# Kernel tuning notes

Measured on AMD Instinct MI355X. Metric: run time of the kernel, lower is better.

The kernel has to match this reference:

```python
import jax, jax.numpy as jnp
import numpy as np

N_WIRES = 22
DEPTH = 1


def _apply_ry(state, theta, wire):
    # RY(theta) = [[cos(t/2), -sin(t/2)], [sin(t/2), cos(t/2)]] (torchquantum convention)
    c = jnp.cos(theta * 0.5).astype(jnp.complex64)
    s = jnp.sin(theta * 0.5).astype(jnp.complex64)
    st = jnp.moveaxis(state, wire, 0)  # [2, 2^(n-1) ...]
    new = jnp.stack([c * st[0] - s * st[1], s * st[0] + c * st[1]])
    return jnp.moveaxis(new, 0, wire)


def _apply_cnot(state, ctrl, tgt):
    st = jnp.moveaxis(state, (ctrl, tgt), (0, 1))
    st = st.at[1].set(st[1, ::-1])  # flip target where control == 1
    return jnp.moveaxis(st, (0, 1), (ctrl, tgt))


def _encode(angles, n_wires=N_WIRES, depth=DEPTH):
    # start in |0...0>
    state = jnp.zeros((2,) * n_wires, dtype=jnp.complex64).at[(0,) * n_wires].set(1.0 + 0.0j)
    for w in range(n_wires):
        state = _apply_ry(state, angles[w], w)
    for _ in range(depth):
        for i in range(n_wires):
            state = _apply_cnot(state, i, (i + 1) % n_wires)
    return state


def setup_inputs() -> dict:
    key = jax.random.key(0)
    kx, ky = jax.random.split(key)
    x = jax.random.normal(kx, (N_WIRES,), dtype=jnp.float32)
    y = jax.random.normal(ky, (N_WIRES,), dtype=jnp.float32)
    return {"x": x, "y": y}


def reference(x, y):
    n = N_WIRES
    psi_x = _encode(x)  # state1 in the torch code
    psi_y = _encode(y)
    # torch does: states_y @ states_x.conj() on tensors of shape [1, 2, ..., 2]
    # -> batched 2x2 matmul over the leading n-1 qubit axes, then abs().view(-1)
    shape = (1,) + (2,) * n
    overlap = jnp.matmul(psi_y.reshape(shape), jnp.conj(psi_x).reshape(shape))
    return jnp.abs(overlap).reshape(-1)
```

## Files before the change

### kernel.cpp

```cpp
#include <hip/hip_runtime.h>
#include <math.h>


#define N_WIRES 22

__global__ __launch_bounds__(256) void quantum_overlap_kernel(
    const float* __restrict__ x, const float* __restrict__ y,
    float* __restrict__ out)
{
    __shared__ float fx[2 * N_WIRES];
    __shared__ float fy[2 * N_WIRES];
    const int t = threadIdx.x;
    if (t < N_WIRES) {
        float sv, cv;
        sincosf(0.5f * x[t], &sv, &cv);
        fx[2 * t] = cv; fx[2 * t + 1] = sv;
        sincosf(0.5f * y[t], &sv, &cv);
        fy[2 * t] = cv; fy[2 * t + 1] = sv;
    }
    __syncthreads();

    const unsigned b = blockIdx.x * 256u + (unsigned)t;

    float coreX = 1.0f, coreY = 1.0f;
#pragma unroll
    for (int k = 2; k <= 19; ++k) {
        unsigned bit = ((b >> (19 - k)) ^ (b >> (20 - k))) & 1u;
        coreX *= fx[2 * k + bit];
        coreY *= fy[2 * k + bit];
    }

    const unsigned s0  = (b >> 19) & 1u;
    const unsigned s1  = (b >> 18) & 1u;
    const unsigned s19 = b & 1u;

    float X[2][2], Y[2][2];
#pragma unroll
    for (int i20 = 0; i20 < 2; ++i20) {
#pragma unroll
        for (int i21 = 0; i21 < 2; ++i21) {
            unsigned a0  = s0 ^ (unsigned)i21;
            unsigned a1  = s1 ^ s0 ^ (unsigned)i21;
            unsigned a20 = (unsigned)i20 ^ s19;
            unsigned a21 = (unsigned)i21 ^ (unsigned)i20;
            float gX = fx[a0] * fx[2 + a1] * fx[40 + a20] * fx[42 + a21];
            float gY = fy[a0] * fy[2 + a1] * fy[40 + a20] * fy[42 + a21];
            X[i20][i21] = coreX * gX;
            Y[i20][i21] = coreY * gY;
        }
    }

    float4 o;
    o.x = fabsf(Y[0][0] * X[0][0] + Y[0][1] * X[1][0]);
    o.y = fabsf(Y[0][0] * X[0][1] + Y[0][1] * X[1][1]);
    o.z = fabsf(Y[1][0] * X[0][0] + Y[1][1] * X[1][0]);
    o.w = fabsf(Y[1][0] * X[0][1] + Y[1][1] * X[1][1]);
    reinterpret_cast<float4*>(out)[b] = o;
}

extern "C" void kernel_launch(void* const* d_in, const int* in_sizes, int n_in,
                              void* d_out, int out_size, void* d_ws, size_t ws_size,
                              hipStream_t stream) {
    const float* x = (const float*)d_in[0];
    const float* y = (const float*)d_in[1];
    float* out = (float*)d_out;
    const unsigned n_b = 1u << 20;
    quantum_overlap_kernel<<<n_b / 256, 256, 0, stream>>>(x, y, out);
}
```

Baseline: 64.38 us.

## Factor product-state amplitudes into precomputed half tables plus 2x2 overlap lookup

Adds a small precompute kernel that builds 512-entry partial-product tables for the two halves of the middle qubits of each state, plus an 8-entry table of the absolute 2x2 overlap factors. The main kernel then forms each output from a Gray-code index, two table lookups per state, and a float4 broadcast, instead of an 18-term product chain plus per-thread gate math. This cuts ALU work in a kernel that writes 16 MB, at the price of an extra launch and a dependency on workspace memory. It also relies on pulling the common core factor out of the absolute value.

Result: no change. 63.95 us (-0.7%).

```diff
diff --git a/kernel.cpp b/kernel.cpp
--- a/kernel.cpp
+++ b/kernel.cpp
@@ -2,59 +2,70 @@
 #include <math.h>
 
 
-#define N_WIRES 22
-
-__global__ __launch_bounds__(256) void quantum_overlap_kernel(
+__global__ __launch_bounds__(256) void qk_precompute(
     const float* __restrict__ x, const float* __restrict__ y,
-    float* __restrict__ out)
+    float* __restrict__ ws)
 {
-    __shared__ float fx[2 * N_WIRES];
-    __shared__ float fy[2 * N_WIRES];
+    __shared__ float f[2][44];
     const int t = threadIdx.x;
-    if (t < N_WIRES) {
+    if (t < 22) {
         float sv, cv;
         sincosf(0.5f * x[t], &sv, &cv);
-        fx[2 * t] = cv; fx[2 * t + 1] = sv;
+        f[0][2 * t] = cv; f[0][2 * t + 1] = sv;
         sincosf(0.5f * y[t], &sv, &cv);
-        fy[2 * t] = cv; fy[2 * t + 1] = sv;
+        f[1][2 * t] = cv; f[1][2 * t + 1] = sv;
     }
     __syncthreads();
 
-    const unsigned b = blockIdx.x * 256u + (unsigned)t;
+    const int e   = blockIdx.x * 256 + t;
+    const int tbl = e >> 9;
+    const int i   = e & 511;
+    const float* F = f[tbl & 1];
+    float prod = 1.0f;
+    if (tbl < 2) {
+#pragma unroll
+        for (int q = 0; q < 9; ++q) prod *= F[2 * (10 - q) + ((i >> q) & 1)];
+    } else {
+#pragma unroll
+        for (int p = 0; p < 9; ++p) prod *= F[2 * (19 - p) + ((i >> p) & 1)];
+    }
+    ws[e] = prod;
 
-    float coreX = 1.0f, coreY = 1.0f;
+    if (blockIdx.x == 0 && t < 8) {
+        const int s0 = (t >> 2) & 1, s1 = (t >> 1) & 1, s19 = t & 1;
 #pragma unroll
-    for (int k = 2; k <= 19; ++k) {
-        unsigned bit = ((b >> (19 - k)) ^ (b >> (20 - k))) & 1u;
-        coreX *= fx[2 * k + bit];
-        coreY *= fy[2 * k + bit];
-    }
-
-    const unsigned s0  = (b >> 19) & 1u;
-    const unsigned s1  = (b >> 18) & 1u;
-    const unsigned s19 = b & 1u;
-
-    float X[2][2], Y[2][2];
+        for (int ii = 0; ii < 2; ++ii) {
 #pragma unroll
-    for (int i20 = 0; i20 < 2; ++i20) {
+            for (int j = 0; j < 2; ++j) {
+                float sum = 0.0f;
 #pragma unroll
-        for (int i21 = 0; i21 < 2; ++i21) {
-            unsigned a0  = s0 ^ (unsigned)i21;
-            unsigned a1  = s1 ^ s0 ^ (unsigned)i21;
-            unsigned a20 = (unsigned)i20 ^ s19;
-            unsigned a21 = (unsigned)i21 ^ (unsigned)i20;
-            float gX = fx[a0] * fx[2 + a1] * fx[40 + a20] * fx[42 + a21];
-            float gY = fy[a0] * fy[2 + a1] * fy[40 + a20] * fy[42 + a21];
-            X[i20][i21] = coreX * gX;
-            Y[i20][i21] = coreY * gY;
+                for (int k = 0; k < 2; ++k) {
+                    float kx = f[0][s0 ^ j] * f[0][2 + (s1 ^ s0 ^ j)]
+                             * f[0][40 + (k ^ s19)] * f[0][42 + (j ^ k)];
+                    float ky = f[1][s0 ^ k] * f[1][2 + (s1 ^ s0 ^ k)]
+                             * f[1][40 + (ii ^ s19)] * f[1][42 + (k ^ ii)];
+                    sum += ky * kx;
+                }
+                ws[2048 + 4 * t + 2 * ii + j] = fabsf(sum);
+            }
         }
     }
+}
 
+__global__ __launch_bounds__(256) void qk_main(
+    const float* __restrict__ ws, float* __restrict__ out)
+{
+    const unsigned b  = blockIdx.x * 256u + threadIdx.x;
+    const unsigned g  = b ^ (b >> 1);
+    const unsigned i2 = g & 511u;
+    const unsigned i1 = (g >> 9) & 511u;
+    const float coreX = ws[i1]        * ws[1024u + i2];
+    const float coreY = ws[512u + i1] * ws[1536u + i2];
+    const float p = fabsf(coreX * coreY);
+    const unsigned m = ((b >> 17) & 6u) | (b & 1u);
+    const float4 a = reinterpret_cast<const float4*>(ws + 2048)[m];
     float4 o;
-    o.x = fabsf(Y[0][0] * X[0][0] + Y[0][1] * X[1][0]);
-    o.y = fabsf(Y[0][0] * X[0][1] + Y[0][1] * X[1][1]);
-    o.z = fabsf(Y[1][0] * X[0][0] + Y[1][1] * X[1][0]);
-    o.w = fabsf(Y[1][0] * X[0][1] + Y[1][1] * X[1][1]);
+    o.x = p * a.x; o.y = p * a.y; o.z = p * a.z; o.w = p * a.w;
     reinterpret_cast<float4*>(out)[b] = o;
 }
 
@@ -63,7 +74,9 @@
                               hipStream_t stream) {
     const float* x = (const float*)d_in[0];
     const float* y = (const float*)d_in[1];
+    float* ws  = (float*)d_ws;
     float* out = (float*)d_out;
+    qk_precompute<<<8, 256, 0, stream>>>(x, y, ws);
     const unsigned n_b = 1u << 20;
-    quantum_overlap_kernel<<<n_b / 256, 256, 0, stream>>>(x, y, out);
+    qk_main<<<n_b / 256, 256, 0, stream>>>(ws, out);
 }
```
